# Kernel tuning notes

Hardware: AMD Instinct MI355X
Metric: run time of the kernel (lower is better)

The kernel has to match this reference:

```python
import jax, jax.numpy as jnp
import numpy as np
from jax.scipy.special import gammaln

# Problem sizes (static)
N = 50000          # nodes
P = 200000         # paths (source->target pairs in the transitive closure)
L = 6              # edges (nodes) per path -> flat edge list length E = P*L
E = P * L
MAX_DELAY = 128
DT = 1.0
T = int(MAX_DELAY * int(1 / DT))   # expanded time window (== 128)
EPS = 1e-12


def gamma_irf(params):
    """IRF_FN entry: per-node gamma (Nash-cascade) impulse response, [N, T]."""
    a = jax.nn.softplus(params[:, 0]) + 1.0      # shape  > 1
    b = jax.nn.softplus(params[:, 1]) + 0.5      # scale  > 0.5
    t = (jnp.arange(T, dtype=jnp.float32) + 0.5) * jnp.float32(DT)  # [T]
    log_irf = ((a[:, None] - 1.0) * jnp.log(t)[None, :]
               - t[None, :] / b[:, None]
               - gammaln(a)[:, None]
               - a[:, None] * jnp.log(b)[:, None])
    return jnp.exp(log_irf) * jnp.float32(DT)    # [N, T]


def setup_inputs() -> dict:
    key = jax.random.key(0)
    k1, k2 = jax.random.split(key)
    params = jax.random.normal(k1, (N, 2), dtype=jnp.float32)
    edges_flat = jax.random.randint(k2, (E,), 0, N, dtype=jnp.int32)
    path_cumsum = jnp.arange(P + 1, dtype=jnp.int32) * L  # segment offsets into edges_flat
    return {"params": params, "edges_flat": edges_flat, "path_cumsum": path_cumsum}


def reference(params, edges_flat, path_cumsum):
    # --- irf_fn + rfft ---------------------------------------------------
    irfs = gamma_irf(params)                          # [N, T]
    irfs_freq = jnp.fft.rfft(irfs, n=T, axis=-1)      # [N, F] complex64

    # --- log_transitive_closure: product of per-edge spectra along paths -
    log_f = jnp.log(irfs_freq + EPS)                  # complex log, [N, F]
    seg_ids = jnp.searchsorted(path_cumsum[1:], jnp.arange(E, dtype=path_cumsum.dtype),
                               side="right")          # [E] path id per flat edge
    path_log = jax.ops.segment_sum(log_f[edges_flat], seg_ids, num_segments=P)  # [P, F]
    path_freq = jnp.exp(path_log)                     # product along path, [P, F]

    # coords: (source node, target node) of each path; include_index_diag appends (i, i)
    src = edges_flat[path_cumsum[:-1]]
    dst = edges_flat[path_cumsum[1:] - 1]
    diag = jnp.arange(N, dtype=edges_flat.dtype)
    coords = jnp.stack([jnp.concatenate([src, diag]),
                        jnp.concatenate([dst, diag])])              # [2, P+N]
    freq_all = jnp.concatenate([path_freq, irfs_freq], axis=0)      # [P+N, F]

    # --- irfft + postprocessing ------------------------------------------
    irfs_agg = jnp.fft.irfft(freq_all, n=T, axis=-1)  # [P+N, T]
    irfs_agg = jax.nn.relu(irfs_agg)
    # sampler.phi_k: avg-pool by factor int(1/dt) == 1 -> identity when dt=1
    irfs_agg = jnp.flip(irfs_agg, axis=-1)
    irfs_agg = irfs_agg / (jnp.sum(irfs_agg, axis=-1, keepdims=True) + EPS)
    # SparseKernel(coords, values, kernel_size=(N, N, T)) -> return its contents
    return (coords, irfs_agg)
```

## Files before the change

### kernel.cpp

```cpp
#include <hip/hip_runtime.h>
#include <hip/hip_bf16.h>

#define N_NODES 50000
#define P_PATHS 200000
#define N_ROWS  250000
#define L_EDGES 6
#define T_LEN   128
#define F_BINS  65
#define EPSF    1e-12f
#define PIF     3.14159265358979323846f
#define COORD_ELEMS ((size_t)2 * (P_PATHS + N_NODES))
#define FREQ_BYTES  ((size_t)N_NODES * F_BINS * 8)
#define KDIM  160
#define KPAD  192
#define KPADN 136
#define ROWS_BLK 64

typedef _Float16 v2h __attribute__((ext_vector_type(2)));
typedef _Float16 v8h __attribute__((ext_vector_type(8)));
typedef float    v4f __attribute__((ext_vector_type(4)));

__device__ __forceinline__ int swzA(int row, int h) {
    return (((h >> 3) ^ (row & 7)) << 3) | (h & 7);
}

__device__ __forceinline__ float softplus_(float x) {
    const float e = __expf(-fabsf(x));
    return fmaxf(x, 0.0f) + __logf(1.0f + e);
}

__device__ __forceinline__ float lgamma_pos_(float x) {
    const float ser = 1.000000000190015f
                    + 76.18009172947146f     / (x + 1.0f)
                    - 86.50532032941677f     / (x + 2.0f)
                    + 24.01409824083091f     / (x + 3.0f)
                    - 1.231739572450155f     / (x + 4.0f)
                    + 0.1208650973866179e-2f / (x + 5.0f)
                    - 0.5395239384953e-5f    / (x + 6.0f);
    const float tmp = x + 5.5f;
    return (x + 0.5f) * __logf(tmp) - tmp + __logf(2.5066282746310005f * ser / x);
}

__global__ void irfa49o_wgen(_Float16* __restrict__ Wt) {
    const int idx = blockIdx.x * 256 + threadIdx.x;
    if (idx >= 128 * KDIM) return;
    const int t  = idx / KDIM;
    const int kk = idx - t * KDIM;
    float val = 0.0f;
    if (kk < 130 && kk != 129) {
        const int j = kk >> 1;
        const int m = (j * t) & 127;
        const float th = (float)m * (PIF / 64.0f);
        const float cj = (j == 0 || j == 64) ? 1.0f : 2.0f;
        const float tri = (kk & 1) ? -__sinf(th) : __cosf(th);
        val = cj * tri * (1.0f / 128.0f);
    }
    Wt[idx] = (_Float16)val;
}

__global__ void irfa49p_freq(const float* __restrict__ params, _Float16* __restrict__ freqh) {
    __shared__ float sx[8][T_LEN];
    __shared__ float su[8][64];
    __shared__ float sv[8][64];
    const int tid  = threadIdx.x;
    const int slot = tid >> 5;
    const int tl   = tid & 31;
    const int n    = blockIdx.x * 8 + slot;
    _Float16* fh   = freqh + (size_t)n * KPADN;

    const float a  = softplus_(params[2 * n + 0]) + 1.0f;
    const float b  = softplus_(params[2 * n + 1]) + 0.5f;
    const float lg = lgamma_pos_(a);
    const float lb = __logf(b);
    const float rb = 1.0f / b;
    const float am1 = a - 1.0f;
    const float cst = -lg - a * lb;

    float S = 0.0f;
    #pragma unroll
    for (int j = 0; j < 4; ++j) {
        const float tc = (float)(tl + 32 * j) + 0.5f;
        const float x  = __expf(fmaf(am1, __logf(tc), fmaf(-tc, rb, cst)));
        sx[slot][tl + 32 * j] = x;
        S += x;
    }

    float s0  = S;
    float s64 = (tl & 1) ? -S : S;
    float c32 = ((tl & 3) == 0) ? S : (((tl & 3) == 2) ? -S : 0.0f);
    float s32 = ((tl & 3) == 1) ? S : (((tl & 3) == 3) ? -S : 0.0f);
    #pragma unroll
    for (int m = 16; m; m >>= 1) {
        s0  += __shfl_xor(s0, m);
        s64 += __shfl_xor(s64, m);
        c32 += __shfl_xor(c32, m);
        s32 += __shfl_xor(s32, m);
    }
    __syncthreads();

    {
        const int i1 = tl + 1;
        const float xa = sx[slot][i1], xb = sx[slot][T_LEN - i1];
        su[slot][i1] = xa + xb;
        sv[slot][i1] = xa - xb;
        if (tl < 31) {
            const int i2 = tl + 33;
            const float xc = sx[slot][i2], xd = sx[slot][T_LEN - i2];
            su[slot][i2] = xc + xd;
            sv[slot][i2] = xc - xd;
        }
    }
    __syncthreads();

    if (tl == 0) {
        v2h h;
        h[0] = (_Float16)s0;  h[1] = (_Float16)0.0f;   *(v2h*)(fh + 0)   = h;
        h[0] = (_Float16)c32; h[1] = (_Float16)(-s32); *(v2h*)(fh + 64)  = h;
        h[0] = (_Float16)s64; h[1] = (_Float16)0.0f;   *(v2h*)(fh + 128) = h;
        h[0] = (_Float16)0.0f; h[1] = (_Float16)0.0f;
        *(v2h*)(fh + 130) = h; *(v2h*)(fh + 132) = h; *(v2h*)(fh + 134) = h;
        return;
    }

    const float x0v  = sx[slot][0];
    const float x64v = sx[slot][64];
    const int   k    = tl;
    const float th   = (float)k * (PIF / 64.0f);
    const float c1 = __cosf(th), s1 = __sinf(th);
    const float c2 = 2.0f * c1 * c1 - 1.0f;
    const float s2 = 2.0f * s1 * c1;
    const float K  = 2.0f * c2;

    float ue1 = 0.0f, ue2 = 0.0f, ve1 = 0.0f, ve2 = 0.0f;
    float uo1 = 0.0f, uo2 = 0.0f, vo1 = 0.0f, vo2 = 0.0f;
    #pragma unroll
    for (int m = 31; m >= 1; --m) {
        const float2 uu = *(const float2*)&su[slot][2 * m];
        const float2 vv = *(const float2*)&sv[slot][2 * m];
        float v0;
        v0 = fmaf(K, ue1, uu.x - ue2); ue2 = ue1; ue1 = v0;
        v0 = fmaf(K, ve1, vv.x - ve2); ve2 = ve1; ve1 = v0;
        v0 = fmaf(K, uo1, uu.y - uo2); uo2 = uo1; uo1 = v0;
        v0 = fmaf(K, vo1, vv.y - vo2); vo2 = vo1; vo1 = v0;
    }
    {
        float v0;
        v0 = fmaf(K, uo1, su[slot][1] - uo2); uo2 = uo1; uo1 = v0;
        v0 = fmaf(K, vo1, sv[slot][1] - vo2); vo2 = vo1; vo1 = v0;
    }

    const float Ec = fmaf(ue1, c2, -ue2);
    const float Es = ve1 * s2;
    const float ReSu = fmaf(-uo2, c2, uo1);
    const float ImSu = uo2 * s2;
    const float Oc   = c1 * ReSu - s1 * ImSu;
    const float ReSv = fmaf(-vo2, c2, vo1);
    const float ImSv = vo2 * s2;
    const float Os   = s1 * ReSv + c1 * ImSv;

    const float base = x0v + ((k & 1) ? -x64v : x64v);
    v2h h;
    h[0] = (_Float16)(base + Ec + Oc);
    h[1] = (_Float16)(-(Es + Os));
    *(v2h*)(fh + 2 * k) = h;
    h[0] = (_Float16)(base + Ec - Oc);
    h[1] = (_Float16)(Es - Os);
    *(v2h*)(fh + 2 * (64 - k)) = h;
}

__global__ __launch_bounds__(256) void irfa49q_paths(const _Float16* __restrict__ freqh,
                                                     const int* __restrict__ edges,
                                                     const _Float16* __restrict__ Wt,
                                                     float* __restrict__ out_agg) {
    __shared__ _Float16 sA[ROWS_BLK * KPAD];
    const int tid   = threadIdx.x;
    const int rbase = blockIdx.x * ROWS_BLK;

    {
        const int slot = tid >> 5;
        const int tl   = tid & 31;
        #pragma unroll
        for (int pass = 0; pass < 8; ++pass) {
            const int rho = pass * 8 + slot;
            const int r   = rbase + rho;
            float p1r = 0.0f, p1i = 0.0f, p2r = 0.0f, p2i = 0.0f, q = 0.0f;
            if (r < P_PATHS) {
                int eidx[L_EDGES];
                const int eb = r * L_EDGES;
                #pragma unroll
                for (int j = 0; j < L_EDGES; ++j) eidx[j] = edges[eb + j];
                v2h av[L_EDGES], bv[L_EDGES];
                _Float16 fq[L_EDGES];
                #pragma unroll
                for (int j = 0; j < L_EDGES; ++j) {
                    const _Float16* fh = freqh + (size_t)eidx[j] * KPADN;
                    av[j] = *(const v2h*)(fh + 2 * tl);
                    bv[j] = *(const v2h*)(fh + 64 + 2 * tl);
                    fq[j] = fh[128];
                }
                p1r = 1.0f; p2r = 1.0f; q = 1.0f;
                #pragma unroll
                for (int j = 0; j < L_EDGES; ++j) {
                    const float ax = (float)av[j][0], ay = (float)av[j][1];
                    float t1 = p1r * ax - p1i * ay;
                    p1i      = p1r * ay + p1i * ax;
                    p1r = t1;
                    const float bx = (float)bv[j][0], by = (float)bv[j][1];
                    float t2 = p2r * bx - p2i * by;
                    p2i      = p2r * by + p2i * bx;
                    p2r = t2;
                    q *= (float)fq[j];
                }
            } else if (r < N_ROWS) {
                const int n = r - P_PATHS;
                const _Float16* fh = freqh + (size_t)n * KPADN;
                const v2h av = *(const v2h*)(fh + 2 * tl);
                const v2h bv = *(const v2h*)(fh + 64 + 2 * tl);
                p1r = (float)av[0]; p1i = (float)av[1];
                p2r = (float)bv[0]; p2i = (float)bv[1];
                q = (float)fh[128];
            }
            _Float16* row = sA + rho * KPAD;
            v2h h;
            h[0] = (_Float16)p1r; h[1] = (_Float16)p1i;
            *(v2h*)&row[swzA(rho, 2 * tl)] = h;
            h[0] = (_Float16)p2r; h[1] = (_Float16)p2i;
            *(v2h*)&row[swzA(rho, 64 + 2 * tl)] = h;
            if (tl == 0) {
                v2h z; z[0] = (_Float16)q; z[1] = (_Float16)0.0f;
                *(v2h*)&row[swzA(rho, 128)] = z;
            }
            if (tl < 31) {
                v2h z; z[0] = (_Float16)0.0f; z[1] = (_Float16)0.0f;
                *(v2h*)&row[swzA(rho, 130 + 2 * tl)] = z;
            }
        }
    }
    __syncthreads();

    const int wv    = tid >> 6;
    const int lane  = tid & 63;
    const int arow  = wv * 16 + (lane & 15);
    const int kgrp  = (lane >> 4) * 8;
    const int tcol  = lane & 15;

    v4f acc[8];
    #pragma unroll
    for (int nt = 0; nt < 8; ++nt) acc[nt] = (v4f){0.0f, 0.0f, 0.0f, 0.0f};

    #pragma unroll
    for (int kt = 0; kt < 5; ++kt) {
        const int kk = kt * 32 + kgrp;
        const v8h afrag = *(const v8h*)&sA[arow * KPAD + swzA(arow, kk)];
        #pragma unroll
        for (int nt = 0; nt < 8; ++nt) {
            const int t = nt * 16 + tcol;
            const v8h bfrag = *(const v8h*)&Wt[t * KDIM + kk];
            acc[nt] = __builtin_amdgcn_mfma_f32_16x16x32_f16(afrag, bfrag, acc[nt], 0, 0, 0);
        }
    }

    const int rgrp = (lane >> 4) * 4;
    #pragma unroll
    for (int reg = 0; reg < 4; ++reg) {
        float vals[8];
        float vsum = 0.0f;
        #pragma unroll
        for (int nt = 0; nt < 8; ++nt) {
            const float v = fmaxf(acc[nt][reg], 0.0f);
            vals[nt] = v;
            vsum += v;
        }
        vsum += __shfl_xor(vsum, 1);
        vsum += __shfl_xor(vsum, 2);
        vsum += __shfl_xor(vsum, 4);
        vsum += __shfl_xor(vsum, 8);
        const int row = rbase + wv * 16 + rgrp + reg;
        if (row < N_ROWS) {
            const float inv = 1.0f / (vsum + EPSF);
            float* op = out_agg + (size_t)row * T_LEN;
            #pragma unroll
            for (int nt = 0; nt < 8; ++nt) {
                const int t = nt * 16 + tcol;
                op[127 - t] = vals[nt] * inv;
            }
        }
    }
}

__global__ void IRFAggregator_39049842655549_kernel(const int* __restrict__ edges,
                                                    float* __restrict__ out) {
    const int M = P_PATHS + N_NODES;
    const int i = blockIdx.x * blockDim.x + threadIdx.x;
    if (i >= 2 * M) return;
    int v;
    if (i < P_PATHS) {
        v = edges[i * L_EDGES];
    } else if (i < M) {
        v = i - P_PATHS;
    } else {
        const int j = i - M;
        if (j < P_PATHS) v = edges[j * L_EDGES + L_EDGES - 1];
        else             v = j - P_PATHS;
    }
    out[i] = (float)v;
}

extern "C" void kernel_launch(void* const* d_in, const int* in_sizes, int n_in,
                              void* d_out, int out_size, void* d_ws, size_t ws_size,
                              hipStream_t stream) {
    const float* params = (const float*)d_in[0];
    const int*   edges  = (const int*)d_in[1];

    _Float16* freqh = (_Float16*)d_ws;
    _Float16* Wt    = (_Float16*)((char*)d_ws + FREQ_BYTES);
    float* out      = (float*)d_out;
    float* out_agg  = out + COORD_ELEMS;

    IRFAggregator_39049842655549_kernel<<<(int)((COORD_ELEMS + 255) / 256), 256, 0, stream>>>(edges, out);
    irfa49o_wgen<<<(128 * KDIM + 255) / 256, 256, 0, stream>>>(Wt);
    irfa49p_freq<<<N_NODES / 8, 256, 0, stream>>>(params, freqh);
    irfa49q_paths<<<(N_ROWS + ROWS_BLK - 1) / ROWS_BLK, 256, 0, stream>>>(freqh, edges, Wt, out_agg);
}
```

Baseline: 131.0 us.

## Pack Nyquist bin into DC imaginary slot to shrink K from 160 to 128

Both DC and Nyquist spectra of a real signal are real, so the Nyquist value is stored in the unused imaginary slot of the DC bin. Each per-node spectrum row then fits in exactly 128 halves. The inverse-DFT matrix, the LDS tile and the MFMA K loop shrink from 5 to 4 steps. This also removes the extra scalar gather per edge and the zero-padding stores. The path product special-cases lane 0 so it multiplies the packed Nyquist value as a real scalar alongside the DC term.

Result: slower. 137.6 us (+5.0%).

```diff
diff --git a/kernel.cpp b/kernel.cpp
--- a/kernel.cpp
+++ b/kernel.cpp
@@ -11,9 +11,8 @@
 #define PIF     3.14159265358979323846f
 #define COORD_ELEMS ((size_t)2 * (P_PATHS + N_NODES))
 #define FREQ_BYTES  ((size_t)N_NODES * F_BINS * 8)
-#define KDIM  160
-#define KPAD  192
-#define KPADN 136
+#define KDIM  128
+#define KPADN 128
 #define ROWS_BLK 64
 
 typedef _Float16 v2h __attribute__((ext_vector_type(2)));
@@ -41,24 +40,25 @@
     return (x + 0.5f) * __logf(tmp) - tmp + __logf(2.5066282746310005f * ser / x);
 }
 
-__global__ void irfa49o_wgen(_Float16* __restrict__ Wt) {
+__global__ void irfa49s_wgen(_Float16* __restrict__ Wt) {
     const int idx = blockIdx.x * 256 + threadIdx.x;
     if (idx >= 128 * KDIM) return;
     const int t  = idx / KDIM;
     const int kk = idx - t * KDIM;
-    float val = 0.0f;
-    if (kk < 130 && kk != 129) {
-        const int j = kk >> 1;
-        const int m = (j * t) & 127;
-        const float th = (float)m * (PIF / 64.0f);
-        const float cj = (j == 0 || j == 64) ? 1.0f : 2.0f;
-        const float tri = (kk & 1) ? -__sinf(th) : __cosf(th);
-        val = cj * tri * (1.0f / 128.0f);
-    }
-    Wt[idx] = (_Float16)val;
-}
-
-__global__ void irfa49p_freq(const float* __restrict__ params, _Float16* __restrict__ freqh) {
+    int j; float cj; bool is_sin;
+    if (kk == 1) { j = 64; cj = 1.0f; is_sin = false; }
+    else {
+        j = kk >> 1;
+        cj = (j == 0) ? 1.0f : 2.0f;
+        is_sin = (kk & 1);
+    }
+    const int m = (j * t) & 127;
+    const float th = (float)m * (PIF / 64.0f);
+    const float tri = is_sin ? -__sinf(th) : __cosf(th);
+    Wt[idx] = (_Float16)(cj * tri * (1.0f / 128.0f));
+}
+
+__global__ void irfa49s_freq(const float* __restrict__ params, _Float16* __restrict__ freqh) {
     __shared__ float sx[8][T_LEN];
     __shared__ float su[8][64];
     __shared__ float sv[8][64];
@@ -114,11 +114,8 @@
 
     if (tl == 0) {
         v2h h;
-        h[0] = (_Float16)s0;  h[1] = (_Float16)0.0f;   *(v2h*)(fh + 0)   = h;
-        h[0] = (_Float16)c32; h[1] = (_Float16)(-s32); *(v2h*)(fh + 64)  = h;
-        h[0] = (_Float16)s64; h[1] = (_Float16)0.0f;   *(v2h*)(fh + 128) = h;
-        h[0] = (_Float16)0.0f; h[1] = (_Float16)0.0f;
-        *(v2h*)(fh + 130) = h; *(v2h*)(fh + 132) = h; *(v2h*)(fh + 134) = h;
+        h[0] = (_Float16)s0;  h[1] = (_Float16)s64;   *(v2h*)(fh + 0)  = h;
+        h[0] = (_Float16)c32; h[1] = (_Float16)(-s32); *(v2h*)(fh + 64) = h;
         return;
     }
 
@@ -168,72 +165,61 @@
     *(v2h*)(fh + 2 * (64 - k)) = h;
 }
 
-__global__ __launch_bounds__(256) void irfa49q_paths(const _Float16* __restrict__ freqh,
+__global__ __launch_bounds__(256) void irfa49s_paths(const _Float16* __restrict__ freqh,
                                                      const int* __restrict__ edges,
                                                      const _Float16* __restrict__ Wt,
                                                      float* __restrict__ out_agg) {
-    __shared__ _Float16 sA[ROWS_BLK * KPAD];
+    __shared__ _Float16 sA[ROWS_BLK * KDIM];
     const int tid   = threadIdx.x;
     const int rbase = blockIdx.x * ROWS_BLK;
-
-    {
-        const int slot = tid >> 5;
-        const int tl   = tid & 31;
-        #pragma unroll
-        for (int pass = 0; pass < 8; ++pass) {
-            const int rho = pass * 8 + slot;
-            const int r   = rbase + rho;
-            float p1r = 0.0f, p1i = 0.0f, p2r = 0.0f, p2i = 0.0f, q = 0.0f;
-            if (r < P_PATHS) {
-                int eidx[L_EDGES];
-                const int eb = r * L_EDGES;
-                #pragma unroll
-                for (int j = 0; j < L_EDGES; ++j) eidx[j] = edges[eb + j];
-                v2h av[L_EDGES], bv[L_EDGES];
-                _Float16 fq[L_EDGES];
-                #pragma unroll
-                for (int j = 0; j < L_EDGES; ++j) {
-                    const _Float16* fh = freqh + (size_t)eidx[j] * KPADN;
-                    av[j] = *(const v2h*)(fh + 2 * tl);
-                    bv[j] = *(const v2h*)(fh + 64 + 2 * tl);
-                    fq[j] = fh[128];
-                }
-                p1r = 1.0f; p2r = 1.0f; q = 1.0f;
-                #pragma unroll
-                for (int j = 0; j < L_EDGES; ++j) {
-                    const float ax = (float)av[j][0], ay = (float)av[j][1];
-                    float t1 = p1r * ax - p1i * ay;
-                    p1i      = p1r * ay + p1i * ax;
-                    p1r = t1;
-                    const float bx = (float)bv[j][0], by = (float)bv[j][1];
-                    float t2 = p2r * bx - p2i * by;
-                    p2i      = p2r * by + p2i * bx;
-                    p2r = t2;
-                    q *= (float)fq[j];
-                }
-            } else if (r < N_ROWS) {
-                const int n = r - P_PATHS;
-                const _Float16* fh = freqh + (size_t)n * KPADN;
-                const v2h av = *(const v2h*)(fh + 2 * tl);
-                const v2h bv = *(const v2h*)(fh + 64 + 2 * tl);
-                p1r = (float)av[0]; p1i = (float)av[1];
-                p2r = (float)bv[0]; p2i = (float)bv[1];
-                q = (float)fh[128];
+    const int slot  = tid >> 5;
+    const int tl    = tid & 31;
+
+    #pragma unroll
+    for (int pass = 0; pass < 8; ++pass) {
+        const int rho = pass * 8 + slot;
+        const int r   = rbase + rho;
+        _Float16* rowp = sA + rho * KDIM;
+        if (r < P_PATHS) {
+            const int eb = r * L_EDGES;
+            v2h av[L_EDGES], bv[L_EDGES];
+            #pragma unroll
+            for (int j = 0; j < L_EDGES; ++j) {
+                const _Float16* fh = freqh + (size_t)edges[eb + j] * KPADN;
+                av[j] = *(const v2h*)(fh + 2 * tl);
+                bv[j] = *(const v2h*)(fh + 64 + 2 * tl);
             }
-            _Float16* row = sA + rho * KPAD;
+            float p1r = 1.0f, p1i = 0.0f, p2r = 1.0f, p2i = 0.0f, q = 1.0f;
+            #pragma unroll
+            for (int j = 0; j < L_EDGES; ++j) {
+                const float ax  = (float)av[j][0];
+                const float ayr = (float)av[j][1];
+                const float ay  = (tl == 0) ? 0.0f : ayr;
+                float t1 = p1r * ax - p1i * ay;
+                p1i      = p1r * ay + p1i * ax;
+                p1r = t1;
+                q *= ayr;
+                const float bx = (float)bv[j][0], by = (float)bv[j][1];
+                float t2 = p2r * bx - p2i * by;
+                p2i      = p2r * by + p2i * bx;
+                p2r = t2;
+            }
             v2h h;
-            h[0] = (_Float16)p1r; h[1] = (_Float16)p1i;
-            *(v2h*)&row[swzA(rho, 2 * tl)] = h;
+            h[0] = (_Float16)p1r;
+            h[1] = (tl == 0) ? (_Float16)q : (_Float16)p1i;
+            *(v2h*)&rowp[swzA(rho, 2 * tl)] = h;
             h[0] = (_Float16)p2r; h[1] = (_Float16)p2i;
-            *(v2h*)&row[swzA(rho, 64 + 2 * tl)] = h;
-            if (tl == 0) {
-                v2h z; z[0] = (_Float16)q; z[1] = (_Float16)0.0f;
-                *(v2h*)&row[swzA(rho, 128)] = z;
+            *(v2h*)&rowp[swzA(rho, 64 + 2 * tl)] = h;
+        } else {
+            v2h av = (v2h){(_Float16)0.0f, (_Float16)0.0f};
+            v2h bv = av;
+            if (r < N_ROWS) {
+                const _Float16* fh = freqh + (size_t)(r - P_PATHS) * KPADN;
+                av = *(const v2h*)(fh + 2 * tl);
+                bv = *(const v2h*)(fh + 64 + 2 * tl);
             }
-            if (tl < 31) {
-                v2h z; z[0] = (_Float16)0.0f; z[1] = (_Float16)0.0f;
-                *(v2h*)&row[swzA(rho, 130 + 2 * tl)] = z;
-            }
+            *(v2h*)&rowp[swzA(rho, 2 * tl)] = av;
+            *(v2h*)&rowp[swzA(rho, 64 + 2 * tl)] = bv;
         }
     }
     __syncthreads();
@@ -249,9 +235,9 @@
     for (int nt = 0; nt < 8; ++nt) acc[nt] = (v4f){0.0f, 0.0f, 0.0f, 0.0f};
 
     #pragma unroll
-    for (int kt = 0; kt < 5; ++kt) {
+    for (int kt = 0; kt < 4; ++kt) {
         const int kk = kt * 32 + kgrp;
-        const v8h afrag = *(const v8h*)&sA[arow * KPAD + swzA(arow, kk)];
+        const v8h afrag = *(const v8h*)&sA[arow * KDIM + swzA(arow, kk)];
         #pragma unroll
         for (int nt = 0; nt < 8; ++nt) {
             const int t = nt * 16 + tcol;
@@ -318,7 +304,7 @@
     float* out_agg  = out + COORD_ELEMS;
 
     IRFAggregator_39049842655549_kernel<<<(int)((COORD_ELEMS + 255) / 256), 256, 0, stream>>>(edges, out);
-    irfa49o_wgen<<<(128 * KDIM + 255) / 256, 256, 0, stream>>>(Wt);
-    irfa49p_freq<<<N_NODES / 8, 256, 0, stream>>>(params, freqh);
-    irfa49q_paths<<<(N_ROWS + ROWS_BLK - 1) / ROWS_BLK, 256, 0, stream>>>(freqh, edges, Wt, out_agg);
-}
+    irfa49s_wgen<<<(128 * KDIM + 255) / 256, 256, 0, stream>>>(Wt);
+    irfa49s_freq<<<N_NODES / 8, 256, 0, stream>>>(params, freqh);
+    irfa49s_paths<<<(N_ROWS + ROWS_BLK - 1) / ROWS_BLK, 256, 0, stream>>>(freqh, edges, Wt, out_agg);
+}
```
